# Kernel tuning notes

Hardware: AMD Instinct MI355X
Metric: run time of the kernel (lower is better)

The kernel has to match this reference:

```python
import jax, jax.numpy as jnp
import numpy as np

EPS = 1e-8  # F.cosine_similarity clamps norms at eps=1e-8


def setup_inputs() -> dict:
    key = jax.random.key(0)
    k1, k2 = jax.random.split(key)
    features = jax.random.normal(k1, (8192, 128), dtype=jnp.float32)
    labels = jax.random.randint(k2, (8192,), 0, 100, dtype=jnp.int64)
    return {"features": features, "labels": labels, "temperature": 0.5}


def reference(features, labels, temperature):
    # Cosine similarity: normalize once, then a single GEMM (same math as the
    # broadcasted F.cosine_similarity, which clamps each norm at EPS).
    norms = jnp.maximum(jnp.linalg.norm(features, axis=1, keepdims=True), EPS)
    f = features / norms                                  # [N, D]
    sim = f @ f.T                                         # [N, N]
    logits = sim / temperature                            # [N, N]

    mask = (labels[:, None] == labels[None, :]).astype(logits.dtype)  # [N, N]
    # Denominator excludes same-label pairs (including the diagonal),
    # exactly as in the torch code: exp(logits) * (1 - mask).
    exp_logits = jnp.exp(logits) * (1.0 - mask)
    log_prob = logits - jnp.log(exp_logits.sum(axis=1, keepdims=True))  # [N, N]

    mean_log_prob_pos = (mask * log_prob).sum(axis=1) / mask.sum(axis=1)  # [N]
    return -mean_log_prob_pos.mean()
```

## Files before the change

kernel.cpp:

```cpp
#include <hip/hip_runtime.h>
#include <hip/hip_bf16.h>

#define N 8192
#define D 128
#define NJS 8
#define NPART (NJS * 2)
#define LN2 0.69314718056f

typedef __bf16 bf16x8 __attribute__((ext_vector_type(8)));
typedef float f32x4 __attribute__((ext_vector_type(4)));
typedef unsigned int u32;

__device__ __forceinline__ void gload_lds16(const void* g, void* l) {
    __builtin_amdgcn_global_load_lds(
        (const __attribute__((address_space(1))) u32*)g,
        (__attribute__((address_space(3))) u32*)l, 16, 0, 0);
}

__global__ void k_norm(const float* __restrict__ feat, const float* __restrict__ tempp,
                       __hip_bfloat16* __restrict__ fbf) {
    const int row  = blockIdx.x * 4 + (threadIdx.x >> 6);
    const int lane = threadIdx.x & 63;
    float2 v = *reinterpret_cast<const float2*>(&feat[row * D + lane * 2]);
    float ss = v.x * v.x + v.y * v.y;
#pragma unroll
    for (int m = 32; m; m >>= 1) ss += __shfl_xor(ss, m);
    const float sc = rsqrtf(tempp[0] * LN2);
    const float r = sc / fmaxf(sqrtf(ss), 1e-8f);
    __hip_bfloat162 o;
    o.x = __float2bfloat16(v.x * r);
    o.y = __float2bfloat16(v.y * r);
    *reinterpret_cast<__hip_bfloat162*>(&fbf[row * D + lane * 2]) = o;
}

__launch_bounds__(256, 2)
__global__ void k_gemm(const __hip_bfloat16* __restrict__ fbf,
                       const int* __restrict__ lab,
                       float* __restrict__ Pspos, float* __restrict__ Pedem) {
    __shared__ char Bs[65536];
    const int ib = blockIdx.x, js = blockIdx.y;
    const int i0 = ib * 128;
    const int tid = threadIdx.x;
    const int wave = tid >> 6, lane = tid & 63;
    const int wm = wave >> 1, wn = wave & 1;
    const int lr = lane & 15, lg = lane >> 4;

    const __hip_bfloat16* pa = fbf + (size_t)(i0 + wm * 64 + lr) * D + lg * 8;
    bf16x8 af[4][4];
#pragma unroll
    for (int mi = 0; mi < 4; ++mi)
#pragma unroll
        for (int ks = 0; ks < 4; ++ks)
            af[mi][ks] = *reinterpret_cast<const bf16x8*>(pa + mi * 16 * D + ks * 32);

    int4 labi[4];
#pragma unroll
    for (int mi = 0; mi < 4; ++mi)
        labi[mi] = *reinterpret_cast<const int4*>(&lab[i0 + wm * 64 + mi * 16 + lg * 4]);

    float rps[4][4] = {}, res_[4][4] = {};

    const char* fbytes = reinterpret_cast<const char*>(fbf);

#define STAGE(t)                                                               \
    {                                                                          \
        const int j0s = js * (NJS * 128) + (t) * 128;                          \
        char* dst = Bs + ((t) & 1) * 32768;                                    \
        _Pragma("unroll")                                                      \
        for (int it = 0; it < 8; ++it) {                                       \
            const int base = (it * 4 + wave) * 64;                             \
            const int c = base + lane;                                         \
            const int row = c >> 4;                                            \
            const int kc = (c & 15) ^ (row & 7);                               \
            gload_lds16(fbytes + (size_t)(j0s + row) * 256 + kc * 16,          \
                        dst + base * 16);                                      \
        }                                                                      \
    }

    STAGE(0);
    __syncthreads();

    for (int t = 0; t < NJS; ++t) {
        if (t < NJS - 1) STAGE(t + 1);
        const char* buf = Bs + (t & 1) * 32768;
        const int j0 = js * (NJS * 128) + t * 128;
#pragma unroll
        for (int h = 0; h < 2; ++h) {
            bf16x8 bfr[2][4];
#pragma unroll
            for (int nih = 0; nih < 2; ++nih)
#pragma unroll
                for (int ks = 0; ks < 4; ++ks) {
                    const int R = wn * 64 + h * 32 + nih * 16 + lr;
                    const int kc = ks * 4 + lg;
                    bfr[nih][ks] = *reinterpret_cast<const bf16x8*>(
                        buf + R * 256 + ((kc ^ (R & 7)) << 4));
                }
            f32x4 acc[4][2] = {};
#pragma unroll
            for (int ks = 0; ks < 4; ++ks)
#pragma unroll
                for (int mi = 0; mi < 4; ++mi)
#pragma unroll
                    for (int nih = 0; nih < 2; ++nih)
                        acc[mi][nih] = __builtin_amdgcn_mfma_f32_16x16x32_bf16(
                            af[mi][ks], bfr[nih][ks], acc[mi][nih], 0, 0, 0);
            int labj[2];
            labj[0] = lab[j0 + wn * 64 + h * 32 + lr];
            labj[1] = lab[j0 + wn * 64 + h * 32 + 16 + lr];
#pragma unroll
            for (int mi = 0; mi < 4; ++mi)
#pragma unroll
                for (int r = 0; r < 4; ++r) {
                    const int li = reinterpret_cast<const int*>(&labi[mi])[r];
#pragma unroll
                    for (int nih = 0; nih < 2; ++nih) {
                        float v = acc[mi][nih][r];
                        bool same = (li == labj[nih]);
                        rps[mi][r]  += same ? v : 0.0f;
                        res_[mi][r] += same ? 0.0f : __builtin_amdgcn_exp2f(v);
                    }
                }
        }
        __syncthreads();
    }

    const int slab = js * 2 + wn;
#pragma unroll
    for (int mi = 0; mi < 4; ++mi)
#pragma unroll
        for (int r = 0; r < 4; ++r) {
            float ps = rps[mi][r], es = res_[mi][r];
#pragma unroll
            for (int m = 1; m < 16; m <<= 1) {
                ps += __shfl_xor(ps, m);
                es += __shfl_xor(es, m);
            }
            if (lr == 0) {
                const int rowl = wm * 64 + mi * 16 + lg * 4 + r;
                Pspos[slab * N + i0 + rowl] = ps;
                Pedem[slab * N + i0 + rowl] = es;
            }
        }
#undef STAGE
}

__global__ void k_tail(const float* __restrict__ Pspos, const float* __restrict__ Pedem,
                       const int* __restrict__ lab, float* __restrict__ out) {
    __shared__ float hist[128];
    __shared__ float wsum[16];
    const int tid = threadIdx.x;
    if (tid < 128) hist[tid] = 0.0f;
    __syncthreads();
#pragma unroll
    for (int k = 0; k < 8; ++k) atomicAdd(&hist[lab[tid + k * 1024]], 1.0f);
    __syncthreads();
    float sum = 0.0f;
#pragma unroll
    for (int k = 0; k < 8; ++k) {
        const int i = tid + k * 1024;
        float sp = 0.0f, ed = 0.0f;
#pragma unroll
        for (int s = 0; s < NPART; ++s) {
            sp += Pspos[s * N + i];
            ed += Pedem[s * N + i];
        }
        const float cnt = hist[lab[i]];
        sum += LN2 * (sp / cnt - __builtin_amdgcn_logf(ed));
    }
#pragma unroll
    for (int m = 32; m; m >>= 1) sum += __shfl_xor(sum, m);
    if ((tid & 63) == 0) wsum[tid >> 6] = sum;
    __syncthreads();
    if (tid < 64) {
        float v = (tid < 16) ? wsum[tid] : 0.0f;
#pragma unroll
        for (int m = 32; m; m >>= 1) v += __shfl_xor(v, m);
        if (tid == 0) out[0] = -(v / (float)N);
    }
}

extern "C" void kernel_launch(void* const* d_in, const int* in_sizes, int n_in,
                              void* d_out, int out_size, void* d_ws, size_t ws_size,
                              hipStream_t stream) {
    const float* feat = (const float*)d_in[0];
    const int* lab    = (const int*)d_in[1];
    const float* temp = (const float*)d_in[2];
    float* out = (float*)d_out;
    char* ws = (char*)d_ws;

    __hip_bfloat16* fbf = (__hip_bfloat16*)ws;
    float* Pspos = (float*)(ws + 2097152);
    float* Pedem = (float*)(ws + 2621440);

    k_norm<<<N / 4, 256, 0, stream>>>(feat, temp, fbf);
    dim3 grid(N / 128, NJS);
    k_gemm<<<grid, 256, 0, stream>>>(fbf, lab, Pspos, Pedem);
    k_tail<<<1, 1024, 0, stream>>>(Pspos, Pedem, lab, out);
}
```

Measured before the change: 61.78 us.

## Exploit symmetry of similarity matrix and parallelize tail reduction

The GEMM now computes only upper-triangular 128x128 tiles of the symmetric similarity matrix and accumulates both row and column partial sums per tile, so each off-diagonal tile serves two row blocks. The LDS double-buffered staging is dropped in favour of direct global loads of a single B tile per block. The single-block tail becomes a 32-block reduction with a last-block-done atomic counter, and k_norm resets that counter. This roughly halves the MFMA and exp work, at the cost of half the grid exiting immediately, wider partial buffers (64 slabs), and an extra cross-wave LDS reduction.

```diff
diff --git a/kernel.cpp b/kernel.cpp
--- a/kernel.cpp
+++ b/kernel.cpp
@@ -3,22 +3,15 @@
 
 #define N 8192
 #define D 128
-#define NJS 8
-#define NPART (NJS * 2)
+#define NSLAB 64
 #define LN2 0.69314718056f
 
 typedef __bf16 bf16x8 __attribute__((ext_vector_type(8)));
 typedef float f32x4 __attribute__((ext_vector_type(4)));
-typedef unsigned int u32;
-
-__device__ __forceinline__ void gload_lds16(const void* g, void* l) {
-    __builtin_amdgcn_global_load_lds(
-        (const __attribute__((address_space(1))) u32*)g,
-        (__attribute__((address_space(3))) u32*)l, 16, 0, 0);
-}
 
 __global__ void k_norm(const float* __restrict__ feat, const float* __restrict__ tempp,
-                       __hip_bfloat16* __restrict__ fbf) {
+                       __hip_bfloat16* __restrict__ fbf, unsigned* __restrict__ counter) {
+    if (blockIdx.x == 0 && threadIdx.x == 0) *counter = 0u;
     const int row  = blockIdx.x * 4 + (threadIdx.x >> 6);
     const int lane = threadIdx.x & 63;
     float2 v = *reinterpret_cast<const float2*>(&feat[row * D + lane * 2]);
@@ -37,9 +30,9 @@
 __global__ void k_gemm(const __hip_bfloat16* __restrict__ fbf,
                        const int* __restrict__ lab,
                        float* __restrict__ Pspos, float* __restrict__ Pedem) {
-    __shared__ char Bs[65536];
-    const int ib = blockIdx.x, js = blockIdx.y;
-    const int i0 = ib * 128;
+    const int b = blockIdx.x, a = blockIdx.y;
+    if (b < a) return;
+    const int i0 = a * 128, j0 = b * 128;
     const int tid = threadIdx.x;
     const int wave = tid >> 6, lane = tid & 63;
     const int wm = wave >> 1, wn = wave & 1;
@@ -59,73 +52,50 @@
         labi[mi] = *reinterpret_cast<const int4*>(&lab[i0 + wm * 64 + mi * 16 + lg * 4]);
 
     float rps[4][4] = {}, res_[4][4] = {};
-
-    const char* fbytes = reinterpret_cast<const char*>(fbf);
-
-#define STAGE(t)                                                               \
-    {                                                                          \
-        const int j0s = js * (NJS * 128) + (t) * 128;                          \
-        char* dst = Bs + ((t) & 1) * 32768;                                    \
-        _Pragma("unroll")                                                      \
-        for (int it = 0; it < 8; ++it) {                                       \
-            const int base = (it * 4 + wave) * 64;                             \
-            const int c = base + lane;                                         \
-            const int row = c >> 4;                                            \
-            const int kc = (c & 15) ^ (row & 7);                               \
-            gload_lds16(fbytes + (size_t)(j0s + row) * 256 + kc * 16,          \
-                        dst + base * 16);                                      \
-        }                                                                      \
-    }
-
-    STAGE(0);
-    __syncthreads();
-
-    for (int t = 0; t < NJS; ++t) {
-        if (t < NJS - 1) STAGE(t + 1);
-        const char* buf = Bs + (t & 1) * 32768;
-        const int j0 = js * (NJS * 128) + t * 128;
-#pragma unroll
-        for (int h = 0; h < 2; ++h) {
-            bf16x8 bfr[2][4];
-#pragma unroll
-            for (int nih = 0; nih < 2; ++nih)
-#pragma unroll
-                for (int ks = 0; ks < 4; ++ks) {
-                    const int R = wn * 64 + h * 32 + nih * 16 + lr;
-                    const int kc = ks * 4 + lg;
-                    bfr[nih][ks] = *reinterpret_cast<const bf16x8*>(
-                        buf + R * 256 + ((kc ^ (R & 7)) << 4));
+    float cps[2][2] = {}, ces[2][2] = {};
+
+#pragma unroll
+    for (int h = 0; h < 2; ++h) {
+        bf16x8 bfr[2][4];
+        int labj[2];
+#pragma unroll
+        for (int nih = 0; nih < 2; ++nih) {
+            const int jrow = j0 + wn * 64 + h * 32 + nih * 16 + lr;
+            const __hip_bfloat16* pb = fbf + (size_t)jrow * D + lg * 8;
+#pragma unroll
+            for (int ks = 0; ks < 4; ++ks)
+                bfr[nih][ks] = *reinterpret_cast<const bf16x8*>(pb + ks * 32);
+            labj[nih] = lab[jrow];
+        }
+        f32x4 acc[4][2] = {};
+#pragma unroll
+        for (int ks = 0; ks < 4; ++ks)
+#pragma unroll
+            for (int mi = 0; mi < 4; ++mi)
+#pragma unroll
+                for (int nih = 0; nih < 2; ++nih)
+                    acc[mi][nih] = __builtin_amdgcn_mfma_f32_16x16x32_bf16(
+                        af[mi][ks], bfr[nih][ks], acc[mi][nih], 0, 0, 0);
+#pragma unroll
+        for (int mi = 0; mi < 4; ++mi)
+#pragma unroll
+            for (int r = 0; r < 4; ++r) {
+                const int li = reinterpret_cast<const int*>(&labi[mi])[r];
+#pragma unroll
+                for (int nih = 0; nih < 2; ++nih) {
+                    const float v = acc[mi][nih][r];
+                    const float e = __builtin_amdgcn_exp2f(v);
+                    const bool same = (li == labj[nih]);
+                    rps[mi][r]    += same ? v : 0.0f;
+                    res_[mi][r]   += same ? 0.0f : e;
+                    cps[h][nih]   += same ? v : 0.0f;
+                    ces[h][nih]   += same ? 0.0f : e;
                 }
-            f32x4 acc[4][2] = {};
-#pragma unroll
-            for (int ks = 0; ks < 4; ++ks)
-#pragma unroll
-                for (int mi = 0; mi < 4; ++mi)
-#pragma unroll
-                    for (int nih = 0; nih < 2; ++nih)
-                        acc[mi][nih] = __builtin_amdgcn_mfma_f32_16x16x32_bf16(
-                            af[mi][ks], bfr[nih][ks], acc[mi][nih], 0, 0, 0);
-            int labj[2];
-            labj[0] = lab[j0 + wn * 64 + h * 32 + lr];
-            labj[1] = lab[j0 + wn * 64 + h * 32 + 16 + lr];
-#pragma unroll
-            for (int mi = 0; mi < 4; ++mi)
-#pragma unroll
-                for (int r = 0; r < 4; ++r) {
-                    const int li = reinterpret_cast<const int*>(&labi[mi])[r];
-#pragma unroll
-                    for (int nih = 0; nih < 2; ++nih) {
-                        float v = acc[mi][nih][r];
-                        bool same = (li == labj[nih]);
-                        rps[mi][r]  += same ? v : 0.0f;
-                        res_[mi][r] += same ? 0.0f : __builtin_amdgcn_exp2f(v);
-                    }
-                }
-        }
-        __syncthreads();
-    }
-
-    const int slab = js * 2 + wn;
+            }
+    }
+
+    __shared__ float redbuf[4][2][128];
+
 #pragma unroll
     for (int mi = 0; mi < 4; ++mi)
 #pragma unroll
@@ -138,45 +108,73 @@
             }
             if (lr == 0) {
                 const int rowl = wm * 64 + mi * 16 + lg * 4 + r;
-                Pspos[slab * N + i0 + rowl] = ps;
-                Pedem[slab * N + i0 + rowl] = es;
-            }
-        }
-#undef STAGE
+                redbuf[0][wn][rowl] = ps;
+                redbuf[1][wn][rowl] = es;
+            }
+        }
+#pragma unroll
+    for (int h = 0; h < 2; ++h)
+#pragma unroll
+        for (int nih = 0; nih < 2; ++nih) {
+            float cp = cps[h][nih], ce = ces[h][nih];
+            cp += __shfl_xor(cp, 16); cp += __shfl_xor(cp, 32);
+            ce += __shfl_xor(ce, 16); ce += __shfl_xor(ce, 32);
+            if (lg == 0) {
+                const int coll = wn * 64 + h * 32 + nih * 16 + lr;
+                redbuf[2][wm][coll] = cp;
+                redbuf[3][wm][coll] = ce;
+            }
+        }
+    __syncthreads();
+
+    if (tid < 128) {
+        const float ps = redbuf[0][0][tid] + redbuf[0][1][tid];
+        const float es = redbuf[1][0][tid] + redbuf[1][1][tid];
+        Pspos[(size_t)b * N + i0 + tid] = ps;
+        Pedem[(size_t)b * N + i0 + tid] = es;
+    } else if (a != b) {
+        const int c = tid - 128;
+        const float cp = redbuf[2][0][c] + redbuf[2][1][c];
+        const float ce = redbuf[3][0][c] + redbuf[3][1][c];
+        Pspos[(size_t)a * N + j0 + c] = cp;
+        Pedem[(size_t)a * N + j0 + c] = ce;
+    }
 }
 
 __global__ void k_tail(const float* __restrict__ Pspos, const float* __restrict__ Pedem,
-                       const int* __restrict__ lab, float* __restrict__ out) {
+                       const int* __restrict__ lab, float* __restrict__ bsums,
+                       unsigned* __restrict__ counter, float* __restrict__ out) {
     __shared__ float hist[128];
-    __shared__ float wsum[16];
+    __shared__ float wsum[4];
     const int tid = threadIdx.x;
     if (tid < 128) hist[tid] = 0.0f;
     __syncthreads();
 #pragma unroll
-    for (int k = 0; k < 8; ++k) atomicAdd(&hist[lab[tid + k * 1024]], 1.0f);
-    __syncthreads();
-    float sum = 0.0f;
-#pragma unroll
-    for (int k = 0; k < 8; ++k) {
-        const int i = tid + k * 1024;
-        float sp = 0.0f, ed = 0.0f;
-#pragma unroll
-        for (int s = 0; s < NPART; ++s) {
-            sp += Pspos[s * N + i];
-            ed += Pedem[s * N + i];
-        }
-        const float cnt = hist[lab[i]];
-        sum += LN2 * (sp / cnt - __builtin_amdgcn_logf(ed));
-    }
-#pragma unroll
-    for (int m = 32; m; m >>= 1) sum += __shfl_xor(sum, m);
-    if ((tid & 63) == 0) wsum[tid >> 6] = sum;
-    __syncthreads();
-    if (tid < 64) {
-        float v = (tid < 16) ? wsum[tid] : 0.0f;
-#pragma unroll
-        for (int m = 32; m; m >>= 1) v += __shfl_xor(v, m);
-        if (tid == 0) out[0] = -(v / (float)N);
+    for (int k = 0; k < 32; ++k) atomicAdd(&hist[lab[tid + k * 256]], 1.0f);
+    __syncthreads();
+
+    const int i = blockIdx.x * 256 + tid;
+    float sp = 0.0f, ed = 0.0f;
+#pragma unroll
+    for (int s = 0; s < NSLAB; ++s) {
+        sp += Pspos[(size_t)s * N + i];
+        ed += Pedem[(size_t)s * N + i];
+    }
+    float term = LN2 * (sp / hist[lab[i]] - __builtin_amdgcn_logf(ed));
+#pragma unroll
+    for (int m = 32; m; m >>= 1) term += __shfl_xor(term, m);
+    if ((tid & 63) == 0) wsum[tid >> 6] = term;
+    __syncthreads();
+    if (tid == 0) {
+        bsums[blockIdx.x] = wsum[0] + wsum[1] + wsum[2] + wsum[3];
+        __threadfence();
+        const unsigned v = atomicAdd(counter, 1u);
+        if (v == 31u) {
+            __threadfence();
+            float t = 0.0f;
+            for (int k = 0; k < 32; ++k) t += bsums[k];
+            out[0] = -(t / (float)N);
+        }
     }
 }
 
@@ -191,10 +189,12 @@
 
     __hip_bfloat16* fbf = (__hip_bfloat16*)ws;
     float* Pspos = (float*)(ws + 2097152);
-    float* Pedem = (float*)(ws + 2621440);
-
-    k_norm<<<N / 4, 256, 0, stream>>>(feat, temp, fbf);
-    dim3 grid(N / 128, NJS);
+    float* Pedem = (float*)(ws + 4194304);
+    float* bsums = (float*)(ws + 6291456);
+    unsigned* counter = (unsigned*)(ws + 6291584);
+
+    k_norm<<<N / 4, 256, 0, stream>>>(feat, temp, fbf, counter);
+    dim3 grid(NSLAB, NSLAB);
     k_gemm<<<grid, 256, 0, stream>>>(fbf, lab, Pspos, Pedem);
-    k_tail<<<1, 1024, 0, stream>>>(Pspos, Pedem, lab, out);
-}
+    k_tail<<<32, 256, 0, stream>>>(Pspos, Pedem, lab, bsums, counter, out);
+}
```

Result: slower. 126.3 us (+104.4%).

## Exploit similarity symmetry and compute positive sums via per-class feature sums

Applied to the files above, without the earlier changes.

The GEMM now processes only the upper-triangular block tiles (544 blocks instead of 512 full tiles covering N×N), producing both row and column partial exp-sums so each off-diagonal tile is computed once. The positive-pair similarity sum is removed from the GEMM and replaced by a dot product of each row with its class's summed normalized features, computed by two new small kernels. The tail is parallelised across 32 blocks with an atomic counter for the final reduction. This aims to roughly halve MFMA and exp work, at the cost of extra launches, a serial per-class scan kernel, and larger partial buffers.

```diff
diff --git a/kernel.cpp b/kernel.cpp
--- a/kernel.cpp
+++ b/kernel.cpp
@@ -3,8 +3,6 @@
 
 #define N 8192
 #define D 128
-#define NJS 8
-#define NPART (NJS * 2)
 #define LN2 0.69314718056f
 
 typedef __bf16 bf16x8 __attribute__((ext_vector_type(8)));
@@ -18,7 +16,8 @@
 }
 
 __global__ void k_norm(const float* __restrict__ feat, const float* __restrict__ tempp,
-                       __hip_bfloat16* __restrict__ fbf) {
+                       __hip_bfloat16* __restrict__ fbf, unsigned* __restrict__ counter) {
+    if (blockIdx.x == 0 && threadIdx.x == 0) *counter = 0u;
     const int row  = blockIdx.x * 4 + (threadIdx.x >> 6);
     const int lane = threadIdx.x & 63;
     float2 v = *reinterpret_cast<const float2*>(&feat[row * D + lane * 2]);
@@ -33,13 +32,56 @@
     *reinterpret_cast<__hip_bfloat162*>(&fbf[row * D + lane * 2]) = o;
 }
 
+__global__ void k_csum(const __hip_bfloat16* __restrict__ fbf, const int* __restrict__ lab,
+                       float* __restrict__ S8, int* __restrict__ cnt8) {
+    const int c = blockIdx.x >> 3, ch = blockIdx.x & 7;
+    const int tid = threadIdx.x;
+    __shared__ int labL[1024];
+#pragma unroll
+    for (int k = 0; k < 8; ++k) labL[tid + k * 128] = lab[ch * 1024 + tid + k * 128];
+    __syncthreads();
+    float s = 0.0f; int cv = 0;
+    for (int j = 0; j < 1024; ++j) {
+        if (labL[j] == c) {
+            s += __bfloat162float(fbf[(size_t)(ch * 1024 + j) * D + tid]);
+            ++cv;
+        }
+    }
+    S8[(size_t)(ch * 100 + c) * 128 + tid] = s;
+    if (tid == 0) cnt8[ch * 100 + c] = cv;
+}
+
+__global__ void k_csum2(const float* __restrict__ S8, const int* __restrict__ cnt8,
+                        float* __restrict__ S, float* __restrict__ cnt) {
+    const int c = blockIdx.x, tid = threadIdx.x;
+    float s = 0.0f;
+#pragma unroll
+    for (int ch = 0; ch < 8; ++ch) s += S8[(size_t)(ch * 100 + c) * 128 + tid];
+    S[(size_t)c * 128 + tid] = s;
+    if (tid == 0) {
+        int cv = 0;
+#pragma unroll
+        for (int ch = 0; ch < 8; ++ch) cv += cnt8[ch * 100 + c];
+        cnt[c] = (float)cv;
+    }
+}
+
 __launch_bounds__(256, 2)
 __global__ void k_gemm(const __hip_bfloat16* __restrict__ fbf,
                        const int* __restrict__ lab,
-                       float* __restrict__ Pspos, float* __restrict__ Pedem) {
+                       float* __restrict__ ProwE, float* __restrict__ PcolE) {
     __shared__ char Bs[65536];
-    const int ib = blockIdx.x, js = blockIdx.y;
-    const int i0 = ib * 128;
+    __shared__ float redC[2][2][128];
+
+    int bid = blockIdx.x, g = 0;
+    while (bid >= 4 * (16 - g)) { bid -= 4 * (16 - g); ++g; }
+    const int na = 16 - g;
+    int a = 4 * g, seg = bid;
+    while (seg >= na) { seg -= na; ++a; }
+    const int bstart = a + seg * 4;
+    const int nt = min(4, 64 - bstart);
+
+    const int i0 = a * 128;
     const int tid = threadIdx.x;
     const int wave = tid >> 6, lane = tid & 63;
     const int wm = wave >> 1, wn = wave & 1;
@@ -58,20 +100,19 @@
     for (int mi = 0; mi < 4; ++mi)
         labi[mi] = *reinterpret_cast<const int4*>(&lab[i0 + wm * 64 + mi * 16 + lg * 4]);
 
-    float rps[4][4] = {}, res_[4][4] = {};
+    float res_[4][4] = {};
 
     const char* fbytes = reinterpret_cast<const char*>(fbf);
-
 #define STAGE(t)                                                               \
     {                                                                          \
-        const int j0s = js * (NJS * 128) + (t) * 128;                          \
+        const int j0s = (bstart + (t)) * 128;                                  \
         char* dst = Bs + ((t) & 1) * 32768;                                    \
         _Pragma("unroll")                                                      \
         for (int it = 0; it < 8; ++it) {                                       \
             const int base = (it * 4 + wave) * 64;                             \
-            const int c = base + lane;                                         \
-            const int row = c >> 4;                                            \
-            const int kc = (c & 15) ^ (row & 7);                               \
+            const int c_ = base + lane;                                        \
+            const int row = c_ >> 4;                                           \
+            const int kc = (c_ & 15) ^ (row & 7);                              \
             gload_lds16(fbytes + (size_t)(j0s + row) * 256 + kc * 16,          \
                         dst + base * 16);                                      \
         }                                                                      \
@@ -80,15 +121,18 @@
     STAGE(0);
     __syncthreads();
 
-    for (int t = 0; t < NJS; ++t) {
-        if (t < NJS - 1) STAGE(t + 1);
+    for (int t = 0; t < nt; ++t) {
+        if (t + 1 < nt) STAGE(t + 1);
         const char* buf = Bs + (t & 1) * 32768;
-        const int j0 = js * (NJS * 128) + t * 128;
+        const int bt = bstart + t;
+        const int j0 = bt * 128;
+        float ces[2][2] = {};
 #pragma unroll
         for (int h = 0; h < 2; ++h) {
             bf16x8 bfr[2][4];
-#pragma unroll
-            for (int nih = 0; nih < 2; ++nih)
+            int labj[2];
+#pragma unroll
+            for (int nih = 0; nih < 2; ++nih) {
 #pragma unroll
                 for (int ks = 0; ks < 4; ++ks) {
                     const int R = wn * 64 + h * 32 + nih * 16 + lr;
@@ -96,6 +140,8 @@
                     bfr[nih][ks] = *reinterpret_cast<const bf16x8*>(
                         buf + R * 256 + ((kc ^ (R & 7)) << 4));
                 }
+                labj[nih] = lab[j0 + wn * 64 + h * 32 + nih * 16 + lr];
+            }
             f32x4 acc[4][2] = {};
 #pragma unroll
             for (int ks = 0; ks < 4; ++ks)
@@ -105,9 +151,6 @@
                     for (int nih = 0; nih < 2; ++nih)
                         acc[mi][nih] = __builtin_amdgcn_mfma_f32_16x16x32_bf16(
                             af[mi][ks], bfr[nih][ks], acc[mi][nih], 0, 0, 0);
-            int labj[2];
-            labj[0] = lab[j0 + wn * 64 + h * 32 + lr];
-            labj[1] = lab[j0 + wn * 64 + h * 32 + 16 + lr];
 #pragma unroll
             for (int mi = 0; mi < 4; ++mi)
 #pragma unroll
@@ -115,68 +158,82 @@
                     const int li = reinterpret_cast<const int*>(&labi[mi])[r];
 #pragma unroll
                     for (int nih = 0; nih < 2; ++nih) {
-                        float v = acc[mi][nih][r];
-                        bool same = (li == labj[nih]);
-                        rps[mi][r]  += same ? v : 0.0f;
-                        res_[mi][r] += same ? 0.0f : __builtin_amdgcn_exp2f(v);
+                        const float e = __builtin_amdgcn_exp2f(acc[mi][nih][r]);
+                        const float em = (li == labj[nih]) ? 0.0f : e;
+                        res_[mi][r] += em;
+                        ces[h][nih] += em;
                     }
                 }
         }
+#pragma unroll
+        for (int h = 0; h < 2; ++h)
+#pragma unroll
+            for (int nih = 0; nih < 2; ++nih) {
+                float ce = ces[h][nih];
+                ce += __shfl_xor(ce, 16);
+                ce += __shfl_xor(ce, 32);
+                if (lg == 0) redC[t & 1][wm][wn * 64 + h * 32 + nih * 16 + lr] = ce;
+            }
         __syncthreads();
-    }
-
-    const int slab = js * 2 + wn;
+        if (tid < 128 && bt != a)
+            PcolE[(size_t)a * N + j0 + tid] = redC[t & 1][0][tid] + redC[t & 1][1][tid];
+    }
+#undef STAGE
+
 #pragma unroll
     for (int mi = 0; mi < 4; ++mi)
 #pragma unroll
         for (int r = 0; r < 4; ++r) {
-            float ps = rps[mi][r], es = res_[mi][r];
-#pragma unroll
-            for (int m = 1; m < 16; m <<= 1) {
-                ps += __shfl_xor(ps, m);
-                es += __shfl_xor(es, m);
-            }
+            float es = res_[mi][r];
+#pragma unroll
+            for (int m = 1; m < 16; m <<= 1) es += __shfl_xor(es, m);
             if (lr == 0) {
                 const int rowl = wm * 64 + mi * 16 + lg * 4 + r;
-                Pspos[slab * N + i0 + rowl] = ps;
-                Pedem[slab * N + i0 + rowl] = es;
+                ProwE[(size_t)(seg * 2 + wn) * N + i0 + rowl] = es;
             }
         }
-#undef STAGE
-}
-
-__global__ void k_tail(const float* __restrict__ Pspos, const float* __restrict__ Pedem,
-                       const int* __restrict__ lab, float* __restrict__ out) {
-    __shared__ float hist[128];
-    __shared__ float wsum[16];
+}
+
+__global__ void k_tail(const float* __restrict__ ProwE, const float* __restrict__ PcolE,
+                       const __hip_bfloat16* __restrict__ fbf, const int* __restrict__ lab,
+                       const float* __restrict__ S, const float* __restrict__ cnt,
+                       float* __restrict__ bsums, unsigned* __restrict__ counter,
+                       float* __restrict__ out) {
     const int tid = threadIdx.x;
-    if (tid < 128) hist[tid] = 0.0f;
+    const int i = blockIdx.x * 256 + tid;
+    const int p = i >> 7;
+    const int c = lab[i];
+    float ed = 0.0f;
+    const int ns = 16 - (p >> 2);
+    for (int s = 0; s < ns; ++s)
+        ed += ProwE[(size_t)(2 * s) * N + i] + ProwE[(size_t)(2 * s + 1) * N + i];
+    for (int aa = 0; aa < p; ++aa)
+        ed += PcolE[(size_t)aa * N + i];
+    float sp = 0.0f;
+    const __hip_bfloat16* fr = fbf + (size_t)i * D;
+    const float* Sc = S + (size_t)c * 128;
+#pragma unroll
+    for (int d = 0; d < 128; d += 8) {
+        bf16x8 v = *reinterpret_cast<const bf16x8*>(fr + d);
+#pragma unroll
+        for (int k = 0; k < 8; ++k) sp += (float)v[k] * Sc[d + k];
+    }
+    float term = LN2 * (sp / cnt[c] - __builtin_amdgcn_logf(ed));
+#pragma unroll
+    for (int m = 32; m; m >>= 1) term += __shfl_xor(term, m);
+    __shared__ float wsum[4];
+    if ((tid & 63) == 0) wsum[tid >> 6] = term;
     __syncthreads();
-#pragma unroll
-    for (int k = 0; k < 8; ++k) atomicAdd(&hist[lab[tid + k * 1024]], 1.0f);
-    __syncthreads();
-    float sum = 0.0f;
-#pragma unroll
-    for (int k = 0; k < 8; ++k) {
-        const int i = tid + k * 1024;
-        float sp = 0.0f, ed = 0.0f;
-#pragma unroll
-        for (int s = 0; s < NPART; ++s) {
-            sp += Pspos[s * N + i];
-            ed += Pedem[s * N + i];
-        }
-        const float cnt = hist[lab[i]];
-        sum += LN2 * (sp / cnt - __builtin_amdgcn_logf(ed));
-    }
-#pragma unroll
-    for (int m = 32; m; m >>= 1) sum += __shfl_xor(sum, m);
-    if ((tid & 63) == 0) wsum[tid >> 6] = sum;
-    __syncthreads();
-    if (tid < 64) {
-        float v = (tid < 16) ? wsum[tid] : 0.0f;
-#pragma unroll
-        for (int m = 32; m; m >>= 1) v += __shfl_xor(v, m);
-        if (tid == 0) out[0] = -(v / (float)N);
+    if (tid == 0) {
+        bsums[blockIdx.x] = wsum[0] + wsum[1] + wsum[2] + wsum[3];
+        __threadfence();
+        const unsigned v = atomicAdd(counter, 1u);
+        if (v == 31u) {
+            __threadfence();
+            float tt = 0.0f;
+            for (int k = 0; k < 32; ++k) tt += bsums[k];
+            out[0] = -(tt / (float)N);
+        }
     }
 }
 
@@ -190,11 +247,18 @@
     char* ws = (char*)d_ws;
 
     __hip_bfloat16* fbf = (__hip_bfloat16*)ws;
-    float* Pspos = (float*)(ws + 2097152);
-    float* Pedem = (float*)(ws + 2621440);
-
-    k_norm<<<N / 4, 256, 0, stream>>>(feat, temp, fbf);
-    dim3 grid(N / 128, NJS);
-    k_gemm<<<grid, 256, 0, stream>>>(fbf, lab, Pspos, Pedem);
-    k_tail<<<1, 1024, 0, stream>>>(Pspos, Pedem, lab, out);
-}
+    float* ProwE = (float*)(ws + 2097152);
+    float* PcolE = (float*)(ws + 3145728);
+    float* S8    = (float*)(ws + 5242880);
+    float* S     = (float*)(ws + 5652480);
+    int*   cnt8  = (int*)  (ws + 5703680);
+    float* cnt   = (float*)(ws + 5706880);
+    float* bsums = (float*)(ws + 5707520);
+    unsigned* counter = (unsigned*)(ws + 5707648);
+
+    k_norm<<<N / 4, 256, 0, stream>>>(feat, temp, fbf, counter);
+    k_csum<<<800, 128, 0, stream>>>(fbf, lab, S8, cnt8);
+    k_csum2<<<100, 128, 0, stream>>>(S8, cnt8, S, cnt);
+    k_gemm<<<544, 256, 0, stream>>>(fbf, lab, ProwE, PcolE);
+    k_tail<<<32, 256, 0, stream>>>(ProwE, PcolE, fbf, lab, S, cnt, bsums, counter, out);
+}
```

Result: slower. 116.1 us (+87.9%).
